# Optimization experiments

Measured on AMD Instinct MI355X. Metric: run time of the kernel, lower is better.

## Reference

```python
import jax, jax.numpy as jnp
import numpy as np


def setup_inputs() -> dict:
    key = jax.random.key(0)
    k1, k2, k3 = jax.random.split(key, 3)
    B, Q, K, D = 4, 2048, 2048, 1024
    query = jax.random.normal(k1, (B, Q, D), dtype=jnp.float32)
    value = jax.random.normal(k2, (B, K, D), dtype=jnp.float32)
    attention_mask = jax.random.randint(k3, (B, Q, K), 0, 2, dtype=jnp.int32)
    return {"query": query, "value": value, "attention_mask": attention_mask}


def reference(query, value, attention_mask):
    # key defaults to value in the original module
    D = query.shape[-1]
    # scores[b,q,k] = sum_d (query[b,q,d] + key[b,k,d])
    #              = rowsum(query)[b,q] + rowsum(key)[b,k]  (separable outer-sum,
    # avoids the (B,Q,K,D) intermediate the torch code materializes)
    q_sum = query.sum(-1)                    # (B, Q)
    k_sum = value.sum(-1)                    # (B, K)  (key == value)
    scores = q_sum[:, :, None] + k_sum[:, None, :]   # (B, Q, K)
    scores = scores / jnp.sqrt(jnp.asarray(D, scores.dtype))  # use_scale=True
    mask_value = -1e9
    scores = scores + (1.0 - attention_mask.astype(scores.dtype)) * mask_value
    attention_weights = jax.nn.softmax(scores, axis=-1)       # (B, Q, K)
    context_vector = jnp.einsum('bqk,bkd->bqd', attention_weights, value)
    return (context_vector, attention_weights)
```

## Files before the change

kernel.cpp:

```cpp
#include <hip/hip_runtime.h>
#include <stdint.h>

#define BB 4
#define QQ 2048
#define KK 2048
#define DD 1024

__device__ inline unsigned short f2bf(float f) {
    unsigned int u = __float_as_uint(f);
    unsigned int r = (u + 0x7fffu + ((u >> 16) & 1u)) >> 16;
    return (unsigned short)r;
}

typedef short bf16x8 __attribute__((ext_vector_type(8)));
typedef float f32x4  __attribute__((ext_vector_type(4)));

__device__ inline void async16(const void* g, void* l) {
    __builtin_amdgcn_global_load_lds(
        (const __attribute__((address_space(1))) unsigned int*)g,
        (__attribute__((address_space(3))) unsigned int*)l,
        16, 0, 0);
}

__global__ __launch_bounds__(256) void rowexp(const float* __restrict__ V,
                                              float* __restrict__ e) {
    int wave = threadIdx.x >> 6, lane = threadIdx.x & 63;
    int row = blockIdx.x * 4 + wave;
    const float* p = V + (size_t)row * DD;
    float s = 0.f;
    for (int j = 0; j < 4; j++) {
        float4 v = *(const float4*)(p + j * 256 + lane * 4);
        s += v.x + v.y + v.z + v.w;
    }
    for (int off = 32; off; off >>= 1) s += __shfl_xor(s, off, 64);
    if (lane == 0) e[row] = __expf(s * 0.03125f);
}

__global__ __launch_bounds__(256) void transpose_conv(const float* __restrict__ V,
                                                      unsigned short* __restrict__ Vt) {
    int bid = blockIdx.x;
    int b  = bid >> 9;
    int r  = bid & 511;
    int kt = r >> 4;
    int dt = r & 15;
    int k0 = kt * 64, d0 = dt * 64;
    __shared__ float tile[64 * 65];
    int t = threadIdx.x;
    for (int i = 0; i < 4; i++) {
        int idx = i * 256 + t;
        int row = idx >> 4;
        int c4  = idx & 15;
        float4 v = *(const float4*)(V + (size_t)(b * KK + k0 + row) * DD + d0 + c4 * 4);
        float* p = &tile[row * 65 + c4 * 4];
        p[0] = v.x; p[1] = v.y; p[2] = v.z; p[3] = v.w;
    }
    __syncthreads();
    for (int i = 0; i < 4; i++) {
        int idx = i * 256 + t;
        int dr = idx >> 4;
        int kc = idx & 15;
        ushort4 o;
        o.x = f2bf(tile[(kc * 4 + 0) * 65 + dr]);
        o.y = f2bf(tile[(kc * 4 + 1) * 65 + dr]);
        o.z = f2bf(tile[(kc * 4 + 2) * 65 + dr]);
        o.w = f2bf(tile[(kc * 4 + 3) * 65 + dr]);
        *(ushort4*)(Vt + (size_t)(b * DD + d0 + dr) * KK + k0 + kc * 4) = o;
    }
}

__global__ __launch_bounds__(256) void weights_k(const int* __restrict__ mask,
                                                 const float* __restrict__ e,
                                                 float* __restrict__ wout,
                                                 unsigned short* __restrict__ wb16) {
    int wave = threadIdx.x >> 6, lane = threadIdx.x & 63;
    int row = blockIdx.x * 4 + wave;
    int b = row >> 11;
    const int4*   mp = (const int4*)(mask + (size_t)row * KK);
    const float4* ep = (const float4*)(e + (size_t)b * KK);
    float4 w[8];
    float s = 0.f;
    for (int j = 0; j < 8; j++) {
        int4   m  = mp[lane + j * 64];
        float4 ev = ep[lane + j * 64];
        w[j].x = m.x ? ev.x : 0.f;
        w[j].y = m.y ? ev.y : 0.f;
        w[j].z = m.z ? ev.z : 0.f;
        w[j].w = m.w ? ev.w : 0.f;
        s += (w[j].x + w[j].y) + (w[j].z + w[j].w);
    }
    for (int off = 32; off; off >>= 1) s += __shfl_xor(s, off, 64);
    float rS = 1.f / s;
    float4*  wp = (float4*)(wout + (size_t)row * KK);
    ushort4* bp = (ushort4*)(wb16 + (size_t)row * KK);
    for (int j = 0; j < 8; j++) {
        float4 v = w[j];
        v.x *= rS; v.y *= rS; v.z *= rS; v.w *= rS;
        wp[lane + j * 64] = v;
        ushort4 pk;
        pk.x = f2bf(v.x); pk.y = f2bf(v.y); pk.z = f2bf(v.z); pk.w = f2bf(v.w);
        bp[lane + j * 64] = pk;
    }
}

__global__ __launch_bounds__(256) void gemm_ctx(const unsigned short* __restrict__ Wb,
                                                const unsigned short* __restrict__ Vt,
                                                float* __restrict__ ctx) {
    int bid = blockIdx.x;
    int dt = bid >> 6;
    int b  = (bid >> 4) & 3;
    int qt = bid & 15;
    int q0 = qt * 128, n0 = dt * 128;
    __shared__ unsigned short As[128 * 64];
    __shared__ unsigned short Bs[128 * 64];
    int tid = threadIdx.x, wave = tid >> 6, lane = tid & 63;
    int quad = lane >> 4, lm = lane & 15;
    int wm = wave >> 1, wn = wave & 1;

    int srow   = lane >> 3;
    int schunk = (lane & 7) ^ srow;
    const unsigned short* Ag = Wb + (size_t)(b * QQ + q0 + wave * 8 + srow) * KK + schunk * 8;
    const unsigned short* Bg = Vt + (size_t)(b * DD + n0 + wave * 8 + srow) * KK + schunk * 8;
    unsigned short* lA = &As[(wave * 8) * 64];
    unsigned short* lB = &Bs[(wave * 8) * 64];

    int m7 = lm & 7;
    int xa0 = lm * 64 + ((0 + quad) ^ m7) * 8;
    int xa1 = lm * 64 + ((4 + quad) ^ m7) * 8;

    f32x4 acc[4][4];
    for (int i = 0; i < 4; i++)
        for (int j = 0; j < 4; j++) acc[i][j] = 0.f;

    for (int k0 = 0; k0 < KK; k0 += 64) {
        if (k0) __syncthreads();
        for (int c = 0; c < 4; c++) {
            async16(Ag + (size_t)(c * 32) * KK + k0, lA + c * 32 * 64);
            async16(Bg + (size_t)(c * 32) * KK + k0, lB + c * 32 * 64);
        }
        __syncthreads();
        bf16x8 a[4][2], bv[4][2];
        for (int i = 0; i < 4; i++) {
            a[i][0]  = *(const bf16x8*)&As[(wm * 64 + i * 16) * 64 + xa0];
            a[i][1]  = *(const bf16x8*)&As[(wm * 64 + i * 16) * 64 + xa1];
            bv[i][0] = *(const bf16x8*)&Bs[(wn * 64 + i * 16) * 64 + xa0];
            bv[i][1] = *(const bf16x8*)&Bs[(wn * 64 + i * 16) * 64 + xa1];
        }
        for (int h = 0; h < 2; h++)
            for (int i = 0; i < 4; i++)
                for (int j = 0; j < 4; j++)
                    acc[i][j] = __builtin_amdgcn_mfma_f32_16x16x32_bf16(a[i][h], bv[j][h], acc[i][j], 0, 0, 0);
    }
    for (int i = 0; i < 4; i++) {
        int rowb = q0 + wm * 64 + i * 16 + quad * 4;
        for (int j = 0; j < 4; j++) {
            int col = n0 + wn * 64 + j * 16 + lm;
            for (int rr = 0; rr < 4; rr++)
                ctx[(size_t)(b * QQ + rowb + rr) * DD + col] = acc[i][j][rr];
        }
    }
}

extern "C" void kernel_launch(void* const* d_in, const int* in_sizes, int n_in,
                              void* d_out, int out_size, void* d_ws, size_t ws_size,
                              hipStream_t stream) {
    const float* value = (const float*)d_in[1];
    const int*   mask  = (const int*)d_in[2];
    float* out = (float*)d_out;

    unsigned short* Vt = (unsigned short*)d_ws;
    unsigned short* Wb = Vt + (size_t)BB * DD * KK;
    float* e = (float*)(Wb + (size_t)BB * QQ * KK);

    float* ctx  = out;
    float* wout = out + (size_t)BB * QQ * DD;

    rowexp<<<(BB * KK) / 4, 256, 0, stream>>>(value, e);
    transpose_conv<<<BB * 512, 256, 0, stream>>>(value, Vt);
    weights_k<<<(BB * QQ) / 4, 256, 0, stream>>>(mask, e, wout, Wb);
    gemm_ctx<<<BB * 128, 256, 0, stream>>>(Wb, Vt, ctx);
}
```

Measured before the change: 243.2 us.

## Fuse key row-sum into transpose and double-buffer GEMM LDS tiles

```diff
diff --git a/kernel.cpp b/kernel.cpp
--- a/kernel.cpp
+++ b/kernel.cpp
@@ -22,22 +22,9 @@
         16, 0, 0);
 }
 
-__global__ __launch_bounds__(256) void rowexp(const float* __restrict__ V,
-                                              float* __restrict__ e) {
-    int wave = threadIdx.x >> 6, lane = threadIdx.x & 63;
-    int row = blockIdx.x * 4 + wave;
-    const float* p = V + (size_t)row * DD;
-    float s = 0.f;
-    for (int j = 0; j < 4; j++) {
-        float4 v = *(const float4*)(p + j * 256 + lane * 4);
-        s += v.x + v.y + v.z + v.w;
-    }
-    for (int off = 32; off; off >>= 1) s += __shfl_xor(s, off, 64);
-    if (lane == 0) e[row] = __expf(s * 0.03125f);
-}
-
-__global__ __launch_bounds__(256) void transpose_conv(const float* __restrict__ V,
-                                                      unsigned short* __restrict__ Vt) {
+__global__ __launch_bounds__(256) void transpose_sum(const float* __restrict__ V,
+                                                     unsigned short* __restrict__ Vt,
+                                                     float* __restrict__ s) {
     int bid = blockIdx.x;
     int b  = bid >> 9;
     int r  = bid & 511;
@@ -53,6 +40,12 @@
         float4 v = *(const float4*)(V + (size_t)(b * KK + k0 + row) * DD + d0 + c4 * 4);
         float* p = &tile[row * 65 + c4 * 4];
         p[0] = v.x; p[1] = v.y; p[2] = v.z; p[3] = v.w;
+        float ps = (v.x + v.y) + (v.z + v.w);
+        ps += __shfl_xor(ps, 8, 16);
+        ps += __shfl_xor(ps, 4, 16);
+        ps += __shfl_xor(ps, 2, 16);
+        ps += __shfl_xor(ps, 1, 16);
+        if (c4 == 0) atomicAdd(s + (size_t)b * KK + k0 + row, ps);
     }
     __syncthreads();
     for (int i = 0; i < 4; i++) {
@@ -69,27 +62,32 @@
 }
 
 __global__ __launch_bounds__(256) void weights_k(const int* __restrict__ mask,
-                                                 const float* __restrict__ e,
+                                                 const float* __restrict__ s,
                                                  float* __restrict__ wout,
                                                  unsigned short* __restrict__ wb16) {
     int wave = threadIdx.x >> 6, lane = threadIdx.x & 63;
     int row = blockIdx.x * 4 + wave;
     int b = row >> 11;
     const int4*   mp = (const int4*)(mask + (size_t)row * KK);
-    const float4* ep = (const float4*)(e + (size_t)b * KK);
+    const float4* ep = (const float4*)(s + (size_t)b * KK);
     float4 w[8];
-    float s = 0.f;
+    float ss = 0.f;
     for (int j = 0; j < 8; j++) {
         int4   m  = mp[lane + j * 64];
-        float4 ev = ep[lane + j * 64];
+        float4 sv = ep[lane + j * 64];
+        float4 ev;
+        ev.x = __expf(sv.x * 0.03125f);
+        ev.y = __expf(sv.y * 0.03125f);
+        ev.z = __expf(sv.z * 0.03125f);
+        ev.w = __expf(sv.w * 0.03125f);
         w[j].x = m.x ? ev.x : 0.f;
         w[j].y = m.y ? ev.y : 0.f;
         w[j].z = m.z ? ev.z : 0.f;
         w[j].w = m.w ? ev.w : 0.f;
-        s += (w[j].x + w[j].y) + (w[j].z + w[j].w);
-    }
-    for (int off = 32; off; off >>= 1) s += __shfl_xor(s, off, 64);
-    float rS = 1.f / s;
+        ss += (w[j].x + w[j].y) + (w[j].z + w[j].w);
+    }
+    for (int off = 32; off; off >>= 1) ss += __shfl_xor(ss, off, 64);
+    float rS = 1.f / ss;
     float4*  wp = (float4*)(wout + (size_t)row * KK);
     ushort4* bp = (ushort4*)(wb16 + (size_t)row * KK);
     for (int j = 0; j < 8; j++) {
@@ -110,8 +108,8 @@
     int b  = (bid >> 4) & 3;
     int qt = bid & 15;
     int q0 = qt * 128, n0 = dt * 128;
-    __shared__ unsigned short As[128 * 64];
-    __shared__ unsigned short Bs[128 * 64];
+    __shared__ unsigned short As[2][128 * 64];
+    __shared__ unsigned short Bs[2][128 * 64];
     int tid = threadIdx.x, wave = tid >> 6, lane = tid & 63;
     int quad = lane >> 4, lm = lane & 15;
     int wm = wave >> 1, wn = wave & 1;
@@ -120,8 +118,10 @@
     int schunk = (lane & 7) ^ srow;
     const unsigned short* Ag = Wb + (size_t)(b * QQ + q0 + wave * 8 + srow) * KK + schunk * 8;
     const unsigned short* Bg = Vt + (size_t)(b * DD + n0 + wave * 8 + srow) * KK + schunk * 8;
-    unsigned short* lA = &As[(wave * 8) * 64];
-    unsigned short* lB = &Bs[(wave * 8) * 64];
+    unsigned short* lA0 = &As[0][(wave * 8) * 64];
+    unsigned short* lA1 = &As[1][(wave * 8) * 64];
+    unsigned short* lB0 = &Bs[0][(wave * 8) * 64];
+    unsigned short* lB1 = &Bs[1][(wave * 8) * 64];
 
     int m7 = lm & 7;
     int xa0 = lm * 64 + ((0 + quad) ^ m7) * 8;
@@ -131,25 +131,50 @@
     for (int i = 0; i < 4; i++)
         for (int j = 0; j < 4; j++) acc[i][j] = 0.f;
 
-    for (int k0 = 0; k0 < KK; k0 += 64) {
-        if (k0) __syncthreads();
-        for (int c = 0; c < 4; c++) {
-            async16(Ag + (size_t)(c * 32) * KK + k0, lA + c * 32 * 64);
-            async16(Bg + (size_t)(c * 32) * KK + k0, lB + c * 32 * 64);
-        }
-        __syncthreads();
-        bf16x8 a[4][2], bv[4][2];
-        for (int i = 0; i < 4; i++) {
-            a[i][0]  = *(const bf16x8*)&As[(wm * 64 + i * 16) * 64 + xa0];
-            a[i][1]  = *(const bf16x8*)&As[(wm * 64 + i * 16) * 64 + xa1];
-            bv[i][0] = *(const bf16x8*)&Bs[(wn * 64 + i * 16) * 64 + xa0];
-            bv[i][1] = *(const bf16x8*)&Bs[(wn * 64 + i * 16) * 64 + xa1];
-        }
-        for (int h = 0; h < 2; h++)
-            for (int i = 0; i < 4; i++)
-                for (int j = 0; j < 4; j++)
-                    acc[i][j] = __builtin_amdgcn_mfma_f32_16x16x32_bf16(a[i][h], bv[j][h], acc[i][j], 0, 0, 0);
-    }
+#define STAGE(dA, dB, kpos) do {                                           \
+        for (int c = 0; c < 4; c++) {                                      \
+            async16(Ag + (size_t)(c * 32) * KK + (kpos), (dA) + c * 32 * 64); \
+            async16(Bg + (size_t)(c * 32) * KK + (kpos), (dB) + c * 32 * 64); \
+        }                                                                  \
+    } while (0)
+
+#define COMPUTE(Ab, Bb) do {                                               \
+        bf16x8 a[4][2], bv[4][2];                                          \
+        for (int i = 0; i < 4; i++) {                                      \
+            a[i][0]  = *(const bf16x8*)&(Ab)[(wm * 64 + i * 16) * 64 + xa0]; \
+            a[i][1]  = *(const bf16x8*)&(Ab)[(wm * 64 + i * 16) * 64 + xa1]; \
+            bv[i][0] = *(const bf16x8*)&(Bb)[(wn * 64 + i * 16) * 64 + xa0]; \
+            bv[i][1] = *(const bf16x8*)&(Bb)[(wn * 64 + i * 16) * 64 + xa1]; \
+        }                                                                  \
+        for (int h = 0; h < 2; h++)                                        \
+            for (int i = 0; i < 4; i++)                                    \
+                for (int j = 0; j < 4; j++)                                \
+                    acc[i][j] = __builtin_amdgcn_mfma_f32_16x16x32_bf16(   \
+                        a[i][h], bv[j][h], acc[i][j], 0, 0, 0);            \
+    } while (0)
+
+#define DRAIN_BARRIER() do {                                               \
+        __builtin_amdgcn_sched_barrier(0);                                 \
+        asm volatile("s_waitcnt vmcnt(0) lgkmcnt(0)" ::: "memory");        \
+        __builtin_amdgcn_s_barrier();                                      \
+    } while (0)
+
+    STAGE(lA0, lB0, 0);
+    DRAIN_BARRIER();
+
+    for (int t = 0; t < 32; t += 2) {
+        STAGE(lA1, lB1, (t + 1) * 64);
+        COMPUTE(&As[0][0], &Bs[0][0]);
+        DRAIN_BARRIER();
+        if (t + 2 < 32) STAGE(lA0, lB0, (t + 2) * 64);
+        COMPUTE(&As[1][0], &Bs[1][0]);
+        if (t + 2 < 32) DRAIN_BARRIER();
+    }
+
+#undef STAGE
+#undef COMPUTE
+#undef DRAIN_BARRIER
+
     for (int i = 0; i < 4; i++) {
         int rowb = q0 + wm * 64 + i * 16 + quad * 4;
         for (int j = 0; j < 4; j++) {
@@ -169,13 +194,13 @@
 
     unsigned short* Vt = (unsigned short*)d_ws;
     unsigned short* Wb = Vt + (size_t)BB * DD * KK;
-    float* e = (float*)(Wb + (size_t)BB * QQ * KK);
+    float* s = (float*)(Wb + (size_t)BB * QQ * KK);
 
     float* ctx  = out;
     float* wout = out + (size_t)BB * QQ * DD;
 
-    rowexp<<<(BB * KK) / 4, 256, 0, stream>>>(value, e);
-    transpose_conv<<<BB * 512, 256, 0, stream>>>(value, Vt);
-    weights_k<<<(BB * QQ) / 4, 256, 0, stream>>>(mask, e, wout, Wb);
+    hipMemsetAsync(s, 0, (size_t)BB * KK * sizeof(float), stream);
+    transpose_sum<<<BB * 512, 256, 0, stream>>>(value, Vt, s);
+    weights_k<<<(BB * QQ) / 4, 256, 0, stream>>>(mask, s, wout, Wb);
     gemm_ctx<<<BB * 128, 256, 0, stream>>>(Wb, Vt, ctx);
 }
```

After: 242.1 us. About the same (-0.5%).
